# Performance work log

Hardware: AMD Instinct MI355X
Metric: run time of the kernel (lower is better)

## Reference

```python
import jax, jax.numpy as jnp
import numpy as np

NUM_NODES = 10000  # fixed by input spec: edge_index values in [0, 10000)


def setup_inputs() -> dict:
    key = jax.random.key(0)
    k1, k2, k3 = jax.random.split(key, 3)
    N, E, D_IN, D_OUT = NUM_NODES, 320000, 256, 256
    x = jax.random.normal(k1, (N, D_IN), dtype=jnp.float32)
    edge_index = jax.random.randint(k2, (2, E), 0, N, dtype=jnp.int64)
    # ensure node N-1 appears so num_nodes == N as in the torch code
    edge_index = edge_index.at[0, 0].set(N - 1)
    # xavier_uniform for [D_IN, D_OUT]
    limit = float(np.sqrt(6.0 / (D_IN + D_OUT)))
    weight = jax.random.uniform(k3, (D_IN, D_OUT), dtype=jnp.float32,
                                minval=-limit, maxval=limit)
    return {"x": x, "edge_index": edge_index, "weight": weight}


def _normalize_adjacency(edge_index, num_nodes):
    src, dst = edge_index[0], edge_index[1]
    ones = jnp.ones(src.shape[0], dtype=jnp.float32)
    # symmetric binarized adjacency: adj[i,j] = adj[j,i] = 1 (set, not add)
    adj = jnp.zeros((num_nodes, num_nodes), dtype=jnp.float32)
    adj = adj.at[src, dst].max(ones)
    adj = adj.at[dst, src].max(ones)
    # one round of self-loops: adj += I
    adj = adj + jnp.eye(num_nodes, dtype=jnp.float32)
    deg = jnp.sum(adj, axis=1)                    # [N]
    dinv = 1.0 / jnp.sqrt(deg)                    # [N]
    # D^-1/2 A D^-1/2 via broadcasting (equivalent to diag mms)
    return adj * dinv[:, None] * dinv[None, :]


def reference(x, edge_index, weight):
    adj = _normalize_adjacency(edge_index, NUM_NODES)  # [N, N]
    h = adj @ x                                        # [N, D_IN]
    return h @ weight                                  # [N, D_OUT]
```

## Files before the change

### kernel.cpp

```cpp
#include <hip/hip_runtime.h>
#include <hip/hip_bf16.h>
#include <stdint.h>

#define N_NODES   10000
#define D_FEAT    256
#define E_EDGES   320000
#define ROW_WORDS 313
#define ROW_STRIDE 320
#define LIST_CAP  1024

#define NB     1000
#define RPB    10
#define B_CAP  1024
#define NBLK_E 313
#define NBLK_W 64
#define NBLK_C 1000
#define NBLK_G 625
#define COLSTR 128

#define LDSTR 264

typedef __attribute__((ext_vector_type(4))) float float4v;
typedef _Float16 half8  __attribute__((ext_vector_type(8)));
typedef _Float16 half4v __attribute__((ext_vector_type(4)));

__device__ __forceinline__ float h2f_lo(uint32_t u) {
    union { uint32_t u; _Float16 h[2]; } v; v.u = u; return (float)v.h[0];
}
__device__ __forceinline__ float h2f_hi(uint32_t u) {
    union { uint32_t u; _Float16 h[2]; } v; v.u = u; return (float)v.h[1];
}


__global__ void __launch_bounds__(1024)
fill_sort(const int* __restrict__ ei, uint32_t* __restrict__ bucketbuf,
          uint32_t* __restrict__ cursors,
          const float* __restrict__ w, _Float16* __restrict__ wt) {
    __shared__ uint32_t hist[1024];
    __shared__ uint32_t lofs[1024];
    __shared__ uint32_t base_s[1024];
    __shared__ uint32_t wsum[16];
    __shared__ uint32_t stage[2048];
    __shared__ uint16_t sbkt[2048];
    int t = threadIdx.x;

    if (blockIdx.x >= NBLK_E) {
        int kb = (blockIdx.x - NBLK_E) * 4;
        int k = kb + (t >> 8), n = t & 255;
        float* st = (float*)stage;
        st[(n << 2) | (t >> 8)] = w[(size_t)k * D_FEAT + n];
        __syncthreads();
        if (t < 256) {
            half4v o = { (_Float16)st[t * 4 + 0], (_Float16)st[t * 4 + 1],
                         (_Float16)st[t * 4 + 2], (_Float16)st[t * 4 + 3] };
            *(half4v*)&wt[(size_t)t * D_FEAT + kb] = o;
        }
        return;
    }

    int wv = t >> 6, lane = t & 63;
    hist[t] = 0;
    __syncthreads();
    int e = blockIdx.x * 1024 + t;
    int b0 = -1, b1 = -1; uint32_t ent0 = 0, ent1 = 0, s0 = 0, s1 = 0;
    if (e < E_EDGES) {
        int s = ei[e], d = ei[E_EDGES + e];
        if ((uint32_t)s < N_NODES && (uint32_t)d < N_NODES) {
            b0 = s / RPB; ent0 = ((uint32_t)(s - b0 * RPB) << 14) | (uint32_t)d;
            b1 = d / RPB; ent1 = ((uint32_t)(d - b1 * RPB) << 14) | (uint32_t)s;
            s0 = atomicAdd(&hist[b0], 1u);
            s1 = atomicAdd(&hist[b1], 1u);
        }
    }
    __syncthreads();
    uint32_t h = hist[t];
    uint32_t incl = h;
    #pragma unroll
    for (int off = 1; off < 64; off <<= 1) {
        uint32_t v = __shfl_up(incl, off, 64);
        if (lane >= off) incl += v;
    }
    if (lane == 63) wsum[wv] = incl;
    __syncthreads();
    if (wv == 0) {
        uint32_t s = (lane < 16) ? wsum[lane] : 0u;
        #pragma unroll
        for (int off = 1; off < 16; off <<= 1) {
            uint32_t v = __shfl_up(s, off, 64);
            if (lane >= off) s += v;
        }
        if (lane < 16) wsum[lane] = s;
    }
    __syncthreads();
    uint32_t wbase = wv ? wsum[wv - 1] : 0u;
    lofs[t] = incl + wbase;
    base_s[t] = h ? atomicAdd(&cursors[t], h) : 0u;
    __syncthreads();
    if (b0 >= 0) {
        uint32_t p0 = lofs[b0] - hist[b0] + s0;
        stage[p0] = ent0; sbkt[p0] = (uint16_t)b0;
        uint32_t p1 = lofs[b1] - hist[b1] + s1;
        stage[p1] = ent1; sbkt[p1] = (uint16_t)b1;
    }
    __syncthreads();
    uint32_t total = lofs[1023];
    for (uint32_t idx = t; idx < total; idx += 1024) {
        uint32_t b = sbkt[idx];
        uint32_t pos = base_s[b] + (idx - (lofs[b] - hist[b]));
        if (pos < B_CAP) bucketbuf[(size_t)b * B_CAP + pos] = stage[idx];
    }
}

__global__ void __launch_bounds__(1024)
csr_gemm(const uint32_t* __restrict__ bucketbuf, const uint32_t* __restrict__ cursors,
         uint32_t* __restrict__ row_deg, float* __restrict__ dinv,
         uint16_t* __restrict__ col,
         const float* __restrict__ x, const _Float16* __restrict__ wt,
         _Float16* __restrict__ yw) {
    __shared__ __align__(16) uint32_t smem[RPB * ROW_WORDS];
    int t = threadIdx.x;

    if (blockIdx.x >= NBLK_C) {
        _Float16* a_lds = (_Float16*)smem;
        int r0 = (blockIdx.x - NBLK_C) * 16;
        int row = t >> 6, c4 = (t & 63) * 4;
        float4v xv = *(const float4v*)(x + (size_t)(r0 + row) * D_FEAT + c4);
        half4v h = { (_Float16)xv[0], (_Float16)xv[1],
                     (_Float16)xv[2], (_Float16)xv[3] };
        *(half4v*)&a_lds[row * LDSTR + c4] = h;
        __syncthreads();
        int wv = t >> 6, lane = t & 63;
        int quad = lane >> 4, r = lane & 15;
        int ct = wv;
        const _Float16* pb = wt + (size_t)(ct * 16 + r) * D_FEAT + quad * 8;
        float4v acc = {0.f, 0.f, 0.f, 0.f};
        #pragma unroll
        for (int kk = 0; kk < D_FEAT; kk += 32) {
            half8 a = *(const half8*)&a_lds[r * LDSTR + kk + quad * 8];
            half8 b = *(const half8*)(pb + kk);
            acc = __builtin_amdgcn_mfma_f32_16x16x32_f16(a, b, acc, 0, 0, 0);
        }
        int colg = ct * 16 + r;
        #pragma unroll
        for (int u = 0; u < 4; u++)
            yw[(size_t)(r0 + quad * 4 + u) * D_FEAT + colg] = (_Float16)acc[u];
        return;
    }

    uint32_t* bm = smem;
    int b = blockIdx.x;
    for (int i = t; i < RPB * ROW_WORDS; i += 1024) bm[i] = 0;
    __syncthreads();
    uint32_t cnt = min(cursors[b], (uint32_t)B_CAP);
    const uint32_t* bb = bucketbuf + (size_t)b * B_CAP;
    for (uint32_t i = t; i < cnt; i += 1024) {
        uint32_t ent = bb[i];
        uint32_t lr = ent >> 14, d = ent & 0x3FFFu;
        atomicOr(&bm[lr * ROW_WORDS + (d >> 5)], 1u << (d & 31));
    }
    __syncthreads();
    int wv = t >> 6, lane = t & 63;
    if (wv < RPB) {
        int r = wv;
        int gi = b * RPB + r;
        uint32_t wb[5]; int tot = 0;
        #pragma unroll
        for (int k = 0; k < 5; k++) {
            int w = lane + 64 * k;
            uint32_t v = (w < ROW_WORDS) ? bm[r * ROW_WORDS + w] : 0u;
            wb[k] = v; tot += __popc(v);
        }
        int incl = tot;
        #pragma unroll
        for (int off = 1; off < 64; off <<= 1) {
            int v = __shfl_up(incl, off, 64);
            if (lane >= off) incl += v;
        }
        uint32_t total = (uint32_t)__shfl(incl, 63, 64);
        if (lane == 0) {
            row_deg[gi] = min(total, (uint32_t)COLSTR);
            dinv[gi]    = 1.0f / sqrtf((float)(total + 1u));
        }
        uint32_t p = (uint32_t)(incl - tot);
        #pragma unroll
        for (int k = 0; k < 5; k++) {
            uint32_t bits = wb[k];
            uint32_t cbase = (uint32_t)(lane + 64 * k) << 5;
            while (bits) {
                if (p < COLSTR)
                    col[(size_t)gi * COLSTR + p] =
                        (uint16_t)(cbase + (uint32_t)__builtin_ctz(bits));
                p++;
                bits &= bits - 1;
            }
        }
    }
}

__global__ void __launch_bounds__(256)
spmm_out(const uint32_t* __restrict__ row_deg, const float* __restrict__ dinv,
         const uint16_t* __restrict__ col, const _Float16* __restrict__ ywp,
         float* __restrict__ out) {
    const uint16_t* yw = (const uint16_t*)ywp;
    int wv = threadIdx.x >> 6, lane = threadIdx.x & 63;
    int half = lane >> 5, sl = lane & 31;
    int i = blockIdx.x * 4 + wv;
    uint32_t base = (uint32_t)i * COLSTR;
    uint32_t deg = min(row_deg[i], (uint32_t)COLSTR);
    float di = dinv[i];
    size_t ch = (size_t)sl * 8;
    float4v z = {0.f, 0.f, 0.f, 0.f};
    float4v accl[8], acch[8];
    #pragma unroll
    for (int k = 0; k < 8; k++) { accl[k] = z; acch[k] = z; }

    uint32_t hb = (uint32_t)(half << 3);
    uint4 cv = {0u, 0u, 0u, 0u};
    if (deg) cv = *(const uint4*)&col[base + hb];

    for (uint32_t t = 0; t < deg; t += 16) {
        uint4 cvn = {0u, 0u, 0u, 0u};
        uint32_t tn = t + 16;
        if (tn < deg) cvn = *(const uint4*)&col[base + tn + hb];
        uint32_t tb = t + hb;
        uint32_t jr[8];
        jr[0] = cv.x & 0xffffu; jr[1] = cv.x >> 16;
        jr[2] = cv.y & 0xffffu; jr[3] = cv.y >> 16;
        jr[4] = cv.z & 0xffffu; jr[5] = cv.z >> 16;
        jr[6] = cv.w & 0xffffu; jr[7] = cv.w >> 16;
        uint4 g[8]; float dk[8];
        #pragma unroll
        for (int k = 0; k < 8; k++) {
            uint32_t j = min(jr[k], (uint32_t)(N_NODES - 1));
            g[k]  = *(const uint4*)(yw + ((size_t)j << 8) + ch);
            dk[k] = dinv[j];
        }
        #pragma unroll
        for (int k = 0; k < 8; k++) {
            float d = (tb + (uint32_t)k < deg) ? dk[k] : 0.f;
            accl[k][0] += d * h2f_lo(g[k].x); accl[k][1] += d * h2f_hi(g[k].x);
            accl[k][2] += d * h2f_lo(g[k].y); accl[k][3] += d * h2f_hi(g[k].y);
            acch[k][0] += d * h2f_lo(g[k].z); acch[k][1] += d * h2f_hi(g[k].z);
            acch[k][2] += d * h2f_lo(g[k].w); acch[k][3] += d * h2f_hi(g[k].w);
        }
        cv = cvn;
    }

    if (half == 0) {
        const uint4 gs = *(const uint4*)(yw + ((size_t)i << 8) + ch);
        accl[0][0] += di * h2f_lo(gs.x); accl[0][1] += di * h2f_hi(gs.x);
        accl[0][2] += di * h2f_lo(gs.y); accl[0][3] += di * h2f_hi(gs.y);
        acch[0][0] += di * h2f_lo(gs.z); acch[0][1] += di * h2f_hi(gs.z);
        acch[0][2] += di * h2f_lo(gs.w); acch[0][3] += di * h2f_hi(gs.w);
    }

    float4v lo = ((accl[0] + accl[1]) + (accl[2] + accl[3])) +
                 ((accl[4] + accl[5]) + (accl[6] + accl[7]));
    float4v hi = ((acch[0] + acch[1]) + (acch[2] + acch[3])) +
                 ((acch[4] + acch[5]) + (acch[6] + acch[7]));
    #pragma unroll
    for (int u = 0; u < 4; u++) {
        lo[u] += __shfl_xor(lo[u], 32, 64);
        hi[u] += __shfl_xor(hi[u], 32, 64);
    }
    float4v res;
    if (half) res = hi; else res = lo;
    float* op = out + (size_t)i * D_FEAT + (size_t)sl * 8 + (half ? 4 : 0);
    *(float4v*)op = di * res;
}


__global__ void scatter_edges_fb(const int* __restrict__ ei,
                                 uint32_t* __restrict__ bitmap) {
    int e = blockIdx.x * blockDim.x + threadIdx.x;
    if (e >= E_EDGES) return;
    int s = ei[e], d = ei[E_EDGES + e];
    if ((uint32_t)s >= N_NODES || (uint32_t)d >= N_NODES) return;
    atomicOr(&bitmap[(size_t)s * ROW_STRIDE + (d >> 5)], 1u << (d & 31));
    atomicOr(&bitmap[(size_t)d * ROW_STRIDE + (s >> 5)], 1u << (s & 31));
}

__global__ void __launch_bounds__(256)
popc_dinv(const uint32_t* __restrict__ bitmap, float* __restrict__ dinv) {
    int wv = threadIdx.x >> 6, lane = threadIdx.x & 63;
    int i = blockIdx.x * 4 + wv;
    const uint32_t* rb = bitmap + (size_t)i * ROW_STRIDE;
    int pop = 0;
    #pragma unroll
    for (int k = 0; k < 5; k++) {
        int w = lane + 64 * k;
        if (w < ROW_WORDS) pop += __popc(rb[w]);
    }
    #pragma unroll
    for (int off = 32; off > 0; off >>= 1) pop += __shfl_xor(pop, off, 64);
    if (lane == 0) dinv[i] = 1.0f / sqrtf((float)(pop + 1));
}

__global__ void __launch_bounds__(256)
spmm_bitmap_fb(const uint32_t* __restrict__ bitmap, const float* __restrict__ dinv,
               const float* __restrict__ xf, float* __restrict__ agg) {
    __shared__ __align__(16) uint32_t lists[4][LIST_CAP];
    int wv = threadIdx.x >> 6, lane = threadIdx.x & 63;
    int i = blockIdx.x * 4 + wv;
    uint32_t* list = lists[wv];
    const uint32_t* rb = bitmap + (size_t)i * ROW_STRIDE;

    uint32_t wbits[5]; int tot = 0;
    #pragma unroll
    for (int k = 0; k < 5; k++) {
        int w = lane + 64 * k;
        uint32_t b = (w < ROW_WORDS) ? rb[w] : 0u;
        wbits[k] = b;
        tot += __popc(b);
    }
    int incl = tot;
    #pragma unroll
    for (int off = 1; off < 64; off <<= 1) {
        int v = __shfl_up(incl, off, 64);
        if (lane >= off) incl += v;
    }
    uint32_t p = (uint32_t)(incl - tot);
    uint32_t deg = (uint32_t)__shfl(incl, 63, 64);
    #pragma unroll
    for (int k = 0; k < 5; k++) {
        uint32_t bits = wbits[k];
        uint32_t base = (uint32_t)(lane + 64 * k) << 5;
        while (bits) {
            if (p < LIST_CAP) list[p] = base + (uint32_t)__builtin_ctz(bits);
            p++;
            bits &= bits - 1;
        }
    }
    if (deg > LIST_CAP) deg = LIST_CAP;

    float di = dinv[i];
    float4v z = {0.f, 0.f, 0.f, 0.f};
    float4v acc0 = z, acc1 = z, acc2 = z, acc3 = z;
    float4v sv = *(const float4v*)(xf + (size_t)i * D_FEAT + lane * 4);
    uint32_t t4 = deg & ~3u;
    for (uint32_t k = 0; k < t4; k += 4) {
        uint4 jv = *(const uint4*)&list[k];
        float d0 = dinv[jv.x], d1 = dinv[jv.y], d2 = dinv[jv.z], d3 = dinv[jv.w];
        float4v v0 = *(const float4v*)(xf + (size_t)jv.x * D_FEAT + lane * 4);
        float4v v1 = *(const float4v*)(xf + (size_t)jv.y * D_FEAT + lane * 4);
        float4v v2 = *(const float4v*)(xf + (size_t)jv.z * D_FEAT + lane * 4);
        float4v v3 = *(const float4v*)(xf + (size_t)jv.w * D_FEAT + lane * 4);
        acc0 += d0 * v0; acc1 += d1 * v1; acc2 += d2 * v2; acc3 += d3 * v3;
    }
    for (uint32_t k = t4; k < deg; k++) {
        uint32_t j = list[k];
        acc0 += dinv[j] * (*(const float4v*)(xf + (size_t)j * D_FEAT + lane * 4));
    }
    float4v acc = (acc0 + acc1) + (acc2 + acc3) + di * sv;
    *(float4v*)(agg + (size_t)i * D_FEAT + lane * 4) = di * acc;
}

__global__ void __launch_bounds__(256)
gemm_valu(float* __restrict__ io, const float* __restrict__ wf) {
    __shared__ __align__(16) float a_lds[16 * D_FEAT];
    int c = threadIdx.x;
    int r0 = blockIdx.x * 16;
    for (int idx = c; idx < 16 * D_FEAT; idx += 256)
        a_lds[idx] = io[(size_t)r0 * D_FEAT + idx];
    __syncthreads();
    float acc[16];
    #pragma unroll
    for (int r = 0; r < 16; r++) acc[r] = 0.f;
    for (int k0 = 0; k0 < D_FEAT; k0 += 4) {
        float w0 = wf[(size_t)(k0 + 0) * D_FEAT + c];
        float w1 = wf[(size_t)(k0 + 1) * D_FEAT + c];
        float w2 = wf[(size_t)(k0 + 2) * D_FEAT + c];
        float w3 = wf[(size_t)(k0 + 3) * D_FEAT + c];
        #pragma unroll
        for (int r = 0; r < 16; r++) {
            float4v av = *(const float4v*)&a_lds[r * D_FEAT + k0];
            acc[r] = fmaf(av[3], w3, fmaf(av[2], w2,
                     fmaf(av[1], w1, fmaf(av[0], w0, acc[r]))));
        }
    }
    #pragma unroll
    for (int r = 0; r < 16; r++)
        io[(size_t)(r0 + r) * D_FEAT + c] = acc[r];
}

extern "C" void kernel_launch(void* const* d_in, const int* in_sizes, int n_in,
                              void* d_out, int out_size, void* d_ws, size_t ws_size,
                              hipStream_t stream) {
    const float* x  = (const float*)d_in[0];
    const int*   ei = (const int*)d_in[1];
    const float* w  = (const float*)d_in[2];
    float* out = (float*)d_out;
    uint8_t* ws = (uint8_t*)d_ws;

    const size_t BB_OFF   = 4096;
    const size_t RD_OFF   = 4100096;
    const size_t DI_OFF   = 4140096;
    const size_t WT_OFF   = 4180096;
    const size_t YW_OFF   = 4311168;
    const size_t COL_OFF  = 9431168;
    const size_t NEED_NEW = 11991168;
    const size_t NEED_FB  = 12840000;

    if (ws_size >= NEED_NEW) {
        uint32_t* cursors   = (uint32_t*)ws;
        uint32_t* bucketbuf = (uint32_t*)(ws + BB_OFF);
        uint32_t* row_deg   = (uint32_t*)(ws + RD_OFF);
        float*    dinv      = (float*)(ws + DI_OFF);
        _Float16* wt        = (_Float16*)(ws + WT_OFF);
        _Float16* yw        = (_Float16*)(ws + YW_OFF);
        uint16_t* col       = (uint16_t*)(ws + COL_OFF);

        hipMemsetAsync(cursors, 0, 4096, stream);
        fill_sort<<<NBLK_E + NBLK_W, 1024, 0, stream>>>(ei, bucketbuf, cursors, w, wt);
        csr_gemm <<<NBLK_C + NBLK_G, 1024, 0, stream>>>(bucketbuf, cursors,
                                                        row_deg, dinv, col, x, wt, yw);
        spmm_out <<<N_NODES / 4, 256, 0, stream>>>(row_deg, dinv, col, yw, out);
    } else if (ws_size >= NEED_FB) {
        uint32_t* bitmap = (uint32_t*)ws;
        float*    dinv   = (float*)(ws + 12800000);

        hipMemsetAsync(bitmap, 0, 12800000, stream);
        scatter_edges_fb<<<(E_EDGES + 255) / 256, 256, 0, stream>>>(ei, bitmap);
        popc_dinv      <<<N_NODES / 4, 256, 0, stream>>>(bitmap, dinv);
        spmm_bitmap_fb <<<N_NODES / 4, 256, 0, stream>>>(bitmap, dinv, x, out);
        gemm_valu      <<<N_NODES / 16, 256, 0, stream>>>(out, w);
    }
}
```

Before: 132.7 us.

## Add bitmap-adjacency path with fused weight cast and MFMA GEMM before SpMM

```diff
diff --git a/kernel.cpp b/kernel.cpp
--- a/kernel.cpp
+++ b/kernel.cpp
@@ -6,7 +6,6 @@
 #define D_FEAT    256
 #define E_EDGES   320000
 #define ROW_WORDS 313
-#define ROW_STRIDE 320
 #define LIST_CAP  1024
 
 #define NB     1000
@@ -29,6 +28,171 @@
 }
 __device__ __forceinline__ float h2f_hi(uint32_t u) {
     union { uint32_t u; _Float16 h[2]; } v; v.u = u; return (float)v.h[1];
+}
+
+
+__global__ void __launch_bounds__(1024)
+scatter_wcast(const int* __restrict__ ei, uint32_t* __restrict__ bitmap,
+              const float* __restrict__ w, _Float16* __restrict__ wt) {
+    __shared__ float st[1024];
+    int t = threadIdx.x;
+
+    if (blockIdx.x >= NBLK_E) {
+        int kb = (blockIdx.x - NBLK_E) * 4;
+        int k = kb + (t >> 8), n = t & 255;
+        st[(n << 2) | (t >> 8)] = w[(size_t)k * D_FEAT + n];
+        __syncthreads();
+        if (t < 256) {
+            half4v o = { (_Float16)st[t * 4 + 0], (_Float16)st[t * 4 + 1],
+                         (_Float16)st[t * 4 + 2], (_Float16)st[t * 4 + 3] };
+            *(half4v*)&wt[(size_t)t * D_FEAT + kb] = o;
+        }
+        return;
+    }
+
+    int e = blockIdx.x * 1024 + t;
+    if (e >= E_EDGES) return;
+    int s = ei[e], d = ei[E_EDGES + e];
+    if ((uint32_t)s >= N_NODES || (uint32_t)d >= N_NODES) return;
+    atomicOr(&bitmap[(size_t)s * ROW_WORDS + (d >> 5)], 1u << (d & 31));
+    atomicOr(&bitmap[(size_t)d * ROW_WORDS + (s >> 5)], 1u << (s & 31));
+}
+
+__global__ void __launch_bounds__(1024)
+gemm_popc(const uint32_t* __restrict__ bitmap, float* __restrict__ dinv,
+          const float* __restrict__ x, const _Float16* __restrict__ wt,
+          _Float16* __restrict__ yw) {
+    __shared__ __align__(16) _Float16 a_lds[16 * LDSTR];
+    int t = threadIdx.x;
+
+    if (blockIdx.x < NBLK_G) {
+        int r0 = blockIdx.x * 16;
+        int row = t >> 6, c4 = (t & 63) * 4;
+        float4v xv = *(const float4v*)(x + (size_t)(r0 + row) * D_FEAT + c4);
+        half4v h = { (_Float16)xv[0], (_Float16)xv[1],
+                     (_Float16)xv[2], (_Float16)xv[3] };
+        *(half4v*)&a_lds[row * LDSTR + c4] = h;
+        __syncthreads();
+        int wv = t >> 6, lane = t & 63;
+        int quad = lane >> 4, r = lane & 15;
+        int ct = wv;
+        const _Float16* pb = wt + (size_t)(ct * 16 + r) * D_FEAT + quad * 8;
+        float4v acc = {0.f, 0.f, 0.f, 0.f};
+        #pragma unroll
+        for (int kk = 0; kk < D_FEAT; kk += 32) {
+            half8 a = *(const half8*)&a_lds[r * LDSTR + kk + quad * 8];
+            half8 b = *(const half8*)(pb + kk);
+            acc = __builtin_amdgcn_mfma_f32_16x16x32_f16(a, b, acc, 0, 0, 0);
+        }
+        int colg = ct * 16 + r;
+        #pragma unroll
+        for (int u = 0; u < 4; u++)
+            yw[(size_t)(r0 + quad * 4 + u) * D_FEAT + colg] = (_Float16)acc[u];
+        return;
+    }
+
+    int wv = t >> 6, lane = t & 63;
+    int i = (blockIdx.x - NBLK_G) * 16 + wv;
+    const uint32_t* rb = bitmap + (size_t)i * ROW_WORDS;
+    int pop = 0;
+    #pragma unroll
+    for (int k = 0; k < 5; k++) {
+        int w = lane + 64 * k;
+        if (w < ROW_WORDS) pop += __popc(rb[w]);
+    }
+    #pragma unroll
+    for (int off = 32; off > 0; off >>= 1) pop += __shfl_xor(pop, off, 64);
+    if (lane == 0) dinv[i] = 1.0f / sqrtf((float)(pop + 1));
+}
+
+__global__ void __launch_bounds__(256)
+spmm_bm(const uint32_t* __restrict__ bitmap, const float* __restrict__ dinv,
+        const _Float16* __restrict__ ywp, float* __restrict__ out) {
+    __shared__ __align__(16) uint32_t lists[4][LIST_CAP];
+    const uint16_t* yw = (const uint16_t*)ywp;
+    int wv = threadIdx.x >> 6, lane = threadIdx.x & 63;
+    int i = blockIdx.x * 4 + wv;
+    uint32_t* list = lists[wv];
+    const uint32_t* rb = bitmap + (size_t)i * ROW_WORDS;
+
+    uint32_t wbits[5]; int tot = 0;
+    #pragma unroll
+    for (int k = 0; k < 5; k++) {
+        int w = lane + 64 * k;
+        uint32_t b = (w < ROW_WORDS) ? rb[w] : 0u;
+        wbits[k] = b;
+        tot += __popc(b);
+    }
+    int incl = tot;
+    #pragma unroll
+    for (int off = 1; off < 64; off <<= 1) {
+        int v = __shfl_up(incl, off, 64);
+        if (lane >= off) incl += v;
+    }
+    uint32_t p = (uint32_t)(incl - tot);
+    uint32_t deg = (uint32_t)__shfl(incl, 63, 64);
+    #pragma unroll
+    for (int k = 0; k < 5; k++) {
+        uint32_t bits = wbits[k];
+        uint32_t cbase = (uint32_t)(lane + 64 * k) << 5;
+        while (bits) {
+            if (p < LIST_CAP) list[p] = cbase + (uint32_t)__builtin_ctz(bits);
+            p++;
+            bits &= bits - 1;
+        }
+    }
+    if (deg > LIST_CAP) deg = LIST_CAP;
+
+    float di = dinv[i];
+    size_t ch = (size_t)lane * 4;
+    float4v z = {0.f, 0.f, 0.f, 0.f};
+    float4v a0 = z, a1 = z, a2 = z, a3 = z, a4 = z, a5 = z, a6 = z, a7 = z;
+    uint32_t t8 = deg & ~7u;
+    uint32_t t = 0;
+    for (; t < t8; t += 8) {
+        uint4 jv0 = *(const uint4*)&list[t];
+        uint4 jv1 = *(const uint4*)&list[t + 4];
+        uint32_t j0 = jv0.x, j1 = jv0.y, j2 = jv0.z, j3 = jv0.w;
+        uint32_t j4 = jv1.x, j5 = jv1.y, j6 = jv1.z, j7 = jv1.w;
+        float d0 = dinv[j0], d1 = dinv[j1], d2 = dinv[j2], d3 = dinv[j3];
+        float d4 = dinv[j4], d5 = dinv[j5], d6 = dinv[j6], d7 = dinv[j7];
+        uint2 g0 = *(const uint2*)(yw + (size_t)j0 * D_FEAT + ch);
+        uint2 g1 = *(const uint2*)(yw + (size_t)j1 * D_FEAT + ch);
+        uint2 g2 = *(const uint2*)(yw + (size_t)j2 * D_FEAT + ch);
+        uint2 g3 = *(const uint2*)(yw + (size_t)j3 * D_FEAT + ch);
+        uint2 g4 = *(const uint2*)(yw + (size_t)j4 * D_FEAT + ch);
+        uint2 g5 = *(const uint2*)(yw + (size_t)j5 * D_FEAT + ch);
+        uint2 g6 = *(const uint2*)(yw + (size_t)j6 * D_FEAT + ch);
+        uint2 g7 = *(const uint2*)(yw + (size_t)j7 * D_FEAT + ch);
+        a0[0] += d0 * h2f_lo(g0.x); a0[1] += d0 * h2f_hi(g0.x);
+        a0[2] += d0 * h2f_lo(g0.y); a0[3] += d0 * h2f_hi(g0.y);
+        a1[0] += d1 * h2f_lo(g1.x); a1[1] += d1 * h2f_hi(g1.x);
+        a1[2] += d1 * h2f_lo(g1.y); a1[3] += d1 * h2f_hi(g1.y);
+        a2[0] += d2 * h2f_lo(g2.x); a2[1] += d2 * h2f_hi(g2.x);
+        a2[2] += d2 * h2f_lo(g2.y); a2[3] += d2 * h2f_hi(g2.y);
+        a3[0] += d3 * h2f_lo(g3.x); a3[1] += d3 * h2f_hi(g3.x);
+        a3[2] += d3 * h2f_lo(g3.y); a3[3] += d3 * h2f_hi(g3.y);
+        a4[0] += d4 * h2f_lo(g4.x); a4[1] += d4 * h2f_hi(g4.x);
+        a4[2] += d4 * h2f_lo(g4.y); a4[3] += d4 * h2f_hi(g4.y);
+        a5[0] += d5 * h2f_lo(g5.x); a5[1] += d5 * h2f_hi(g5.x);
+        a5[2] += d5 * h2f_lo(g5.y); a5[3] += d5 * h2f_hi(g5.y);
+        a6[0] += d6 * h2f_lo(g6.x); a6[1] += d6 * h2f_hi(g6.x);
+        a6[2] += d6 * h2f_lo(g6.y); a6[3] += d6 * h2f_hi(g6.y);
+        a7[0] += d7 * h2f_lo(g7.x); a7[1] += d7 * h2f_hi(g7.x);
+        a7[2] += d7 * h2f_lo(g7.y); a7[3] += d7 * h2f_hi(g7.y);
+    }
+    for (; t < deg; t++) {
+        uint32_t j = list[t];
+        float dj = dinv[j];
+        uint2 g = *(const uint2*)(yw + (size_t)j * D_FEAT + ch);
+        a0[0] += dj * h2f_lo(g.x); a0[1] += dj * h2f_hi(g.x);
+        a0[2] += dj * h2f_lo(g.y); a0[3] += dj * h2f_hi(g.y);
+    }
+    uint2 gs = *(const uint2*)(yw + (size_t)i * D_FEAT + ch);
+    a1[0] += di * h2f_lo(gs.x); a1[1] += di * h2f_hi(gs.x);
+    a1[2] += di * h2f_lo(gs.y); a1[3] += di * h2f_hi(gs.y);
+    float4v acc = ((a0 + a1) + (a2 + a3)) + ((a4 + a5) + (a6 + a7));
+    *(float4v*)(out + (size_t)i * D_FEAT + ch) = di * acc;
 }
 
 
@@ -269,120 +433,6 @@
     *(float4v*)op = di * res;
 }
 
-
-__global__ void scatter_edges_fb(const int* __restrict__ ei,
-                                 uint32_t* __restrict__ bitmap) {
-    int e = blockIdx.x * blockDim.x + threadIdx.x;
-    if (e >= E_EDGES) return;
-    int s = ei[e], d = ei[E_EDGES + e];
-    if ((uint32_t)s >= N_NODES || (uint32_t)d >= N_NODES) return;
-    atomicOr(&bitmap[(size_t)s * ROW_STRIDE + (d >> 5)], 1u << (d & 31));
-    atomicOr(&bitmap[(size_t)d * ROW_STRIDE + (s >> 5)], 1u << (s & 31));
-}
-
-__global__ void __launch_bounds__(256)
-popc_dinv(const uint32_t* __restrict__ bitmap, float* __restrict__ dinv) {
-    int wv = threadIdx.x >> 6, lane = threadIdx.x & 63;
-    int i = blockIdx.x * 4 + wv;
-    const uint32_t* rb = bitmap + (size_t)i * ROW_STRIDE;
-    int pop = 0;
-    #pragma unroll
-    for (int k = 0; k < 5; k++) {
-        int w = lane + 64 * k;
-        if (w < ROW_WORDS) pop += __popc(rb[w]);
-    }
-    #pragma unroll
-    for (int off = 32; off > 0; off >>= 1) pop += __shfl_xor(pop, off, 64);
-    if (lane == 0) dinv[i] = 1.0f / sqrtf((float)(pop + 1));
-}
-
-__global__ void __launch_bounds__(256)
-spmm_bitmap_fb(const uint32_t* __restrict__ bitmap, const float* __restrict__ dinv,
-               const float* __restrict__ xf, float* __restrict__ agg) {
-    __shared__ __align__(16) uint32_t lists[4][LIST_CAP];
-    int wv = threadIdx.x >> 6, lane = threadIdx.x & 63;
-    int i = blockIdx.x * 4 + wv;
-    uint32_t* list = lists[wv];
-    const uint32_t* rb = bitmap + (size_t)i * ROW_STRIDE;
-
-    uint32_t wbits[5]; int tot = 0;
-    #pragma unroll
-    for (int k = 0; k < 5; k++) {
-        int w = lane + 64 * k;
-        uint32_t b = (w < ROW_WORDS) ? rb[w] : 0u;
-        wbits[k] = b;
-        tot += __popc(b);
-    }
-    int incl = tot;
-    #pragma unroll
-    for (int off = 1; off < 64; off <<= 1) {
-        int v = __shfl_up(incl, off, 64);
-        if (lane >= off) incl += v;
-    }
-    uint32_t p = (uint32_t)(incl - tot);
-    uint32_t deg = (uint32_t)__shfl(incl, 63, 64);
-    #pragma unroll
-    for (int k = 0; k < 5; k++) {
-        uint32_t bits = wbits[k];
-        uint32_t base = (uint32_t)(lane + 64 * k) << 5;
-        while (bits) {
-            if (p < LIST_CAP) list[p] = base + (uint32_t)__builtin_ctz(bits);
-            p++;
-            bits &= bits - 1;
-        }
-    }
-    if (deg > LIST_CAP) deg = LIST_CAP;
-
-    float di = dinv[i];
-    float4v z = {0.f, 0.f, 0.f, 0.f};
-    float4v acc0 = z, acc1 = z, acc2 = z, acc3 = z;
-    float4v sv = *(const float4v*)(xf + (size_t)i * D_FEAT + lane * 4);
-    uint32_t t4 = deg & ~3u;
-    for (uint32_t k = 0; k < t4; k += 4) {
-        uint4 jv = *(const uint4*)&list[k];
-        float d0 = dinv[jv.x], d1 = dinv[jv.y], d2 = dinv[jv.z], d3 = dinv[jv.w];
-        float4v v0 = *(const float4v*)(xf + (size_t)jv.x * D_FEAT + lane * 4);
-        float4v v1 = *(const float4v*)(xf + (size_t)jv.y * D_FEAT + lane * 4);
-        float4v v2 = *(const float4v*)(xf + (size_t)jv.z * D_FEAT + lane * 4);
-        float4v v3 = *(const float4v*)(xf + (size_t)jv.w * D_FEAT + lane * 4);
-        acc0 += d0 * v0; acc1 += d1 * v1; acc2 += d2 * v2; acc3 += d3 * v3;
-    }
-    for (uint32_t k = t4; k < deg; k++) {
-        uint32_t j = list[k];
-        acc0 += dinv[j] * (*(const float4v*)(xf + (size_t)j * D_FEAT + lane * 4));
-    }
-    float4v acc = (acc0 + acc1) + (acc2 + acc3) + di * sv;
-    *(float4v*)(agg + (size_t)i * D_FEAT + lane * 4) = di * acc;
-}
-
-__global__ void __launch_bounds__(256)
-gemm_valu(float* __restrict__ io, const float* __restrict__ wf) {
-    __shared__ __align__(16) float a_lds[16 * D_FEAT];
-    int c = threadIdx.x;
-    int r0 = blockIdx.x * 16;
-    for (int idx = c; idx < 16 * D_FEAT; idx += 256)
-        a_lds[idx] = io[(size_t)r0 * D_FEAT + idx];
-    __syncthreads();
-    float acc[16];
-    #pragma unroll
-    for (int r = 0; r < 16; r++) acc[r] = 0.f;
-    for (int k0 = 0; k0 < D_FEAT; k0 += 4) {
-        float w0 = wf[(size_t)(k0 + 0) * D_FEAT + c];
-        float w1 = wf[(size_t)(k0 + 1) * D_FEAT + c];
-        float w2 = wf[(size_t)(k0 + 2) * D_FEAT + c];
-        float w3 = wf[(size_t)(k0 + 3) * D_FEAT + c];
-        #pragma unroll
-        for (int r = 0; r < 16; r++) {
-            float4v av = *(const float4v*)&a_lds[r * D_FEAT + k0];
-            acc[r] = fmaf(av[3], w3, fmaf(av[2], w2,
-                     fmaf(av[1], w1, fmaf(av[0], w0, acc[r]))));
-        }
-    }
-    #pragma unroll
-    for (int r = 0; r < 16; r++)
-        io[(size_t)(r0 + r) * D_FEAT + c] = acc[r];
-}
-
 extern "C" void kernel_launch(void* const* d_in, const int* in_sizes, int n_in,
                               void* d_out, int out_size, void* d_ws, size_t ws_size,
                               hipStream_t stream) {
@@ -392,16 +442,30 @@
     float* out = (float*)d_out;
     uint8_t* ws = (uint8_t*)d_ws;
 
+    const size_t T1_DI   = 12520000;
+    const size_t T1_WT   = 12560000;
+    const size_t T1_YW   = 12691072;
+    const size_t NEED_T1 = 17811072;
+
     const size_t BB_OFF   = 4096;
     const size_t RD_OFF   = 4100096;
     const size_t DI_OFF   = 4140096;
     const size_t WT_OFF   = 4180096;
     const size_t YW_OFF   = 4311168;
     const size_t COL_OFF  = 9431168;
-    const size_t NEED_NEW = 11991168;
-    const size_t NEED_FB  = 12840000;
-
-    if (ws_size >= NEED_NEW) {
+    const size_t NEED_T2  = 11991168;
+
+    if (ws_size >= NEED_T1) {
+        uint32_t* bitmap = (uint32_t*)ws;
+        float*    dinv   = (float*)(ws + T1_DI);
+        _Float16* wt     = (_Float16*)(ws + T1_WT);
+        _Float16* yw     = (_Float16*)(ws + T1_YW);
+
+        hipMemsetAsync(bitmap, 0, 12520000, stream);
+        scatter_wcast<<<NBLK_E + NBLK_W, 1024, 0, stream>>>(ei, bitmap, w, wt);
+        gemm_popc    <<<NBLK_G + 625, 1024, 0, stream>>>(bitmap, dinv, x, wt, yw);
+        spmm_bm      <<<N_NODES / 4, 256, 0, stream>>>(bitmap, dinv, yw, out);
+    } else if (ws_size >= NEED_T2) {
         uint32_t* cursors   = (uint32_t*)ws;
         uint32_t* bucketbuf = (uint32_t*)(ws + BB_OFF);
         uint32_t* row_deg   = (uint32_t*)(ws + RD_OFF);
@@ -415,14 +479,5 @@
         csr_gemm <<<NBLK_C + NBLK_G, 1024, 0, stream>>>(bucketbuf, cursors,
                                                         row_deg, dinv, col, x, wt, yw);
         spmm_out <<<N_NODES / 4, 256, 0, stream>>>(row_deg, dinv, col, yw, out);
-    } else if (ws_size >= NEED_FB) {
-        uint32_t* bitmap = (uint32_t*)ws;
-        float*    dinv   = (float*)(ws + 12800000);
-
-        hipMemsetAsync(bitmap, 0, 12800000, stream);
-        scatter_edges_fb<<<(E_EDGES + 255) / 256, 256, 0, stream>>>(ei, bitmap);
-        popc_dinv      <<<N_NODES / 4, 256, 0, stream>>>(bitmap, dinv);
-        spmm_bitmap_fb <<<N_NODES / 4, 256, 0, stream>>>(bitmap, dinv, x, out);
-        gemm_valu      <<<N_NODES / 16, 256, 0, stream>>>(out, w);
-    }
-}
+    }
+}
```

Measured after the change: 140.4 us. +5.8%, slower.

## Move X·W GEMM blocks into the sort kernel and split out weight cast

Applied to the files above, without the earlier changes.

```diff
diff --git a/kernel.cpp b/kernel.cpp
--- a/kernel.cpp
+++ b/kernel.cpp
@@ -6,16 +6,13 @@
 #define D_FEAT    256
 #define E_EDGES   320000
 #define ROW_WORDS 313
-#define ROW_STRIDE 320
-#define LIST_CAP  1024
 
 #define NB     1000
 #define RPB    10
 #define B_CAP  1024
 #define NBLK_E 313
-#define NBLK_W 64
+#define NBLK_G 625
 #define NBLK_C 1000
-#define NBLK_G 625
 #define COLSTR 128
 
 #define LDSTR 264
@@ -33,32 +30,62 @@
 
 
 __global__ void __launch_bounds__(1024)
-fill_sort(const int* __restrict__ ei, uint32_t* __restrict__ bucketbuf,
+wcast_k(const float* __restrict__ w, _Float16* __restrict__ wt) {
+    __shared__ float st[1024];
+    int t = threadIdx.x;
+    int kb = blockIdx.x * 4;
+    int k = kb + (t >> 8), n = t & 255;
+    st[(n << 2) | (t >> 8)] = w[(size_t)k * D_FEAT + n];
+    __syncthreads();
+    if (t < 256) {
+        half4v o = { (_Float16)st[t * 4 + 0], (_Float16)st[t * 4 + 1],
+                     (_Float16)st[t * 4 + 2], (_Float16)st[t * 4 + 3] };
+        *(half4v*)&wt[(size_t)t * D_FEAT + kb] = o;
+    }
+}
+
+__global__ void __launch_bounds__(1024)
+sort_gemm(const int* __restrict__ ei, uint32_t* __restrict__ bucketbuf,
           uint32_t* __restrict__ cursors,
-          const float* __restrict__ w, _Float16* __restrict__ wt) {
-    __shared__ uint32_t hist[1024];
-    __shared__ uint32_t lofs[1024];
-    __shared__ uint32_t base_s[1024];
-    __shared__ uint32_t wsum[16];
-    __shared__ uint32_t stage[2048];
-    __shared__ uint16_t sbkt[2048];
+          const float* __restrict__ x, const _Float16* __restrict__ wt,
+          _Float16* __restrict__ yw) {
+    __shared__ __align__(16) uint8_t smraw[24640];
     int t = threadIdx.x;
+    int wv = t >> 6, lane = t & 63;
 
     if (blockIdx.x >= NBLK_E) {
-        int kb = (blockIdx.x - NBLK_E) * 4;
-        int k = kb + (t >> 8), n = t & 255;
-        float* st = (float*)stage;
-        st[(n << 2) | (t >> 8)] = w[(size_t)k * D_FEAT + n];
+        _Float16* a_lds = (_Float16*)smraw;
+        int r0 = (blockIdx.x - NBLK_E) * 16;
+        int row = t >> 6, c4 = (t & 63) * 4;
+        float4v xv = *(const float4v*)(x + (size_t)(r0 + row) * D_FEAT + c4);
+        half4v h = { (_Float16)xv[0], (_Float16)xv[1],
+                     (_Float16)xv[2], (_Float16)xv[3] };
+        *(half4v*)&a_lds[row * LDSTR + c4] = h;
         __syncthreads();
-        if (t < 256) {
-            half4v o = { (_Float16)st[t * 4 + 0], (_Float16)st[t * 4 + 1],
-                         (_Float16)st[t * 4 + 2], (_Float16)st[t * 4 + 3] };
-            *(half4v*)&wt[(size_t)t * D_FEAT + kb] = o;
-        }
+        int quad = lane >> 4, r = lane & 15;
+        int ct = wv;
+        const _Float16* pb = wt + (size_t)(ct * 16 + r) * D_FEAT + quad * 8;
+        float4v acc = {0.f, 0.f, 0.f, 0.f};
+        #pragma unroll
+        for (int kk = 0; kk < D_FEAT; kk += 32) {
+            half8 a = *(const half8*)&a_lds[r * LDSTR + kk + quad * 8];
+            half8 b = *(const half8*)(pb + kk);
+            acc = __builtin_amdgcn_mfma_f32_16x16x32_f16(a, b, acc, 0, 0, 0);
+        }
+        int colg = ct * 16 + r;
+        #pragma unroll
+        for (int u = 0; u < 4; u++)
+            yw[(size_t)(r0 + quad * 4 + u) * D_FEAT + colg] = (_Float16)acc[u];
         return;
     }
 
-    int wv = t >> 6, lane = t & 63;
+    uint32_t* hist   = (uint32_t*)(smraw);
+    uint32_t* lofs   = (uint32_t*)(smraw + 4096);
+    uint32_t* base_s = (uint32_t*)(smraw + 8192);
+    uint32_t* wsum   = (uint32_t*)(smraw + 12288);
+    uint32_t* stage  = (uint32_t*)(smraw + 12352);
+    uint16_t* sbkt   = (uint16_t*)(smraw + 20544);
+
     hist[t] = 0;
     __syncthreads();
     int e = blockIdx.x * 1024 + t;
@@ -112,42 +139,11 @@
 }
 
 __global__ void __launch_bounds__(1024)
-csr_gemm(const uint32_t* __restrict__ bucketbuf, const uint32_t* __restrict__ cursors,
+csr_only(const uint32_t* __restrict__ bucketbuf, const uint32_t* __restrict__ cursors,
          uint32_t* __restrict__ row_deg, float* __restrict__ dinv,
-         uint16_t* __restrict__ col,
-         const float* __restrict__ x, const _Float16* __restrict__ wt,
-         _Float16* __restrict__ yw) {
-    __shared__ __align__(16) uint32_t smem[RPB * ROW_WORDS];
+         uint16_t* __restrict__ col) {
+    __shared__ __align__(16) uint32_t bm[RPB * ROW_WORDS];
     int t = threadIdx.x;
-
-    if (blockIdx.x >= NBLK_C) {
-        _Float16* a_lds = (_Float16*)smem;
-        int r0 = (blockIdx.x - NBLK_C) * 16;
-        int row = t >> 6, c4 = (t & 63) * 4;
-        float4v xv = *(const float4v*)(x + (size_t)(r0 + row) * D_FEAT + c4);
-        half4v h = { (_Float16)xv[0], (_Float16)xv[1],
-                     (_Float16)xv[2], (_Float16)xv[3] };
-        *(half4v*)&a_lds[row * LDSTR + c4] = h;
-        __syncthreads();
-        int wv = t >> 6, lane = t & 63;
-        int quad = lane >> 4, r = lane & 15;
-        int ct = wv;
-        const _Float16* pb = wt + (size_t)(ct * 16 + r) * D_FEAT + quad * 8;
-        float4v acc = {0.f, 0.f, 0.f, 0.f};
-        #pragma unroll
-        for (int kk = 0; kk < D_FEAT; kk += 32) {
-            half8 a = *(const half8*)&a_lds[r * LDSTR + kk + quad * 8];
-            half8 b = *(const half8*)(pb + kk);
-            acc = __builtin_amdgcn_mfma_f32_16x16x32_f16(a, b, acc, 0, 0, 0);
-        }
-        int colg = ct * 16 + r;
-        #pragma unroll
-        for (int u = 0; u < 4; u++)
-            yw[(size_t)(r0 + quad * 4 + u) * D_FEAT + colg] = (_Float16)acc[u];
-        return;
-    }
-
-    uint32_t* bm = smem;
     int b = blockIdx.x;
     for (int i = t; i < RPB * ROW_WORDS; i += 1024) bm[i] = 0;
     __syncthreads();
@@ -269,120 +265,6 @@
     *(float4v*)op = di * res;
 }
 
-
-__global__ void scatter_edges_fb(const int* __restrict__ ei,
-                                 uint32_t* __restrict__ bitmap) {
-    int e = blockIdx.x * blockDim.x + threadIdx.x;
-    if (e >= E_EDGES) return;
-    int s = ei[e], d = ei[E_EDGES + e];
-    if ((uint32_t)s >= N_NODES || (uint32_t)d >= N_NODES) return;
-    atomicOr(&bitmap[(size_t)s * ROW_STRIDE + (d >> 5)], 1u << (d & 31));
-    atomicOr(&bitmap[(size_t)d * ROW_STRIDE + (s >> 5)], 1u << (s & 31));
-}
-
-__global__ void __launch_bounds__(256)
-popc_dinv(const uint32_t* __restrict__ bitmap, float* __restrict__ dinv) {
-    int wv = threadIdx.x >> 6, lane = threadIdx.x & 63;
-    int i = blockIdx.x * 4 + wv;
-    const uint32_t* rb = bitmap + (size_t)i * ROW_STRIDE;
-    int pop = 0;
-    #pragma unroll
-    for (int k = 0; k < 5; k++) {
-        int w = lane + 64 * k;
-        if (w < ROW_WORDS) pop += __popc(rb[w]);
-    }
-    #pragma unroll
-    for (int off = 32; off > 0; off >>= 1) pop += __shfl_xor(pop, off, 64);
-    if (lane == 0) dinv[i] = 1.0f / sqrtf((float)(pop + 1));
-}
-
-__global__ void __launch_bounds__(256)
-spmm_bitmap_fb(const uint32_t* __restrict__ bitmap, const float* __restrict__ dinv,
-               const float* __restrict__ xf, float* __restrict__ agg) {
-    __shared__ __align__(16) uint32_t lists[4][LIST_CAP];
-    int wv = threadIdx.x >> 6, lane = threadIdx.x & 63;
-    int i = blockIdx.x * 4 + wv;
-    uint32_t* list = lists[wv];
-    const uint32_t* rb = bitmap + (size_t)i * ROW_STRIDE;
-
-    uint32_t wbits[5]; int tot = 0;
-    #pragma unroll
-    for (int k = 0; k < 5; k++) {
-        int w = lane + 64 * k;
-        uint32_t b = (w < ROW_WORDS) ? rb[w] : 0u;
-        wbits[k] = b;
-        tot += __popc(b);
-    }
-    int incl = tot;
-    #pragma unroll
-    for (int off = 1; off < 64; off <<= 1) {
-        int v = __shfl_up(incl, off, 64);
-        if (lane >= off) incl += v;
-    }
-    uint32_t p = (uint32_t)(incl - tot);
-    uint32_t deg = (uint32_t)__shfl(incl, 63, 64);
-    #pragma unroll
-    for (int k = 0; k < 5; k++) {
-        uint32_t bits = wbits[k];
-        uint32_t base = (uint32_t)(lane + 64 * k) << 5;
-        while (bits) {
-            if (p < LIST_CAP) list[p] = base + (uint32_t)__builtin_ctz(bits);
-            p++;
-            bits &= bits - 1;
-        }
-    }
-    if (deg > LIST_CAP) deg = LIST_CAP;
-
-    float di = dinv[i];
-    float4v z = {0.f, 0.f, 0.f, 0.f};
-    float4v acc0 = z, acc1 = z, acc2 = z, acc3 = z;
-    float4v sv = *(const float4v*)(xf + (size_t)i * D_FEAT + lane * 4);
-    uint32_t t4 = deg & ~3u;
-    for (uint32_t k = 0; k < t4; k += 4) {
-        uint4 jv = *(const uint4*)&list[k];
-        float d0 = dinv[jv.x], d1 = dinv[jv.y], d2 = dinv[jv.z], d3 = dinv[jv.w];
-        float4v v0 = *(const float4v*)(xf + (size_t)jv.x * D_FEAT + lane * 4);
-        float4v v1 = *(const float4v*)(xf + (size_t)jv.y * D_FEAT + lane * 4);
-        float4v v2 = *(const float4v*)(xf + (size_t)jv.z * D_FEAT + lane * 4);
-        float4v v3 = *(const float4v*)(xf + (size_t)jv.w * D_FEAT + lane * 4);
-        acc0 += d0 * v0; acc1 += d1 * v1; acc2 += d2 * v2; acc3 += d3 * v3;
-    }
-    for (uint32_t k = t4; k < deg; k++) {
-        uint32_t j = list[k];
-        acc0 += dinv[j] * (*(const float4v*)(xf + (size_t)j * D_FEAT + lane * 4));
-    }
-    float4v acc = (acc0 + acc1) + (acc2 + acc3) + di * sv;
-    *(float4v*)(agg + (size_t)i * D_FEAT + lane * 4) = di * acc;
-}
-
-__global__ void __launch_bounds__(256)
-gemm_valu(float* __restrict__ io, const float* __restrict__ wf) {
-    __shared__ __align__(16) float a_lds[16 * D_FEAT];
-    int c = threadIdx.x;
-    int r0 = blockIdx.x * 16;
-    for (int idx = c; idx < 16 * D_FEAT; idx += 256)
-        a_lds[idx] = io[(size_t)r0 * D_FEAT + idx];
-    __syncthreads();
-    float acc[16];
-    #pragma unroll
-    for (int r = 0; r < 16; r++) acc[r] = 0.f;
-    for (int k0 = 0; k0 < D_FEAT; k0 += 4) {
-        float w0 = wf[(size_t)(k0 + 0) * D_FEAT + c];
-        float w1 = wf[(size_t)(k0 + 1) * D_FEAT + c];
-        float w2 = wf[(size_t)(k0 + 2) * D_FEAT + c];
-        float w3 = wf[(size_t)(k0 + 3) * D_FEAT + c];
-        #pragma unroll
-        for (int r = 0; r < 16; r++) {
-            float4v av = *(const float4v*)&a_lds[r * D_FEAT + k0];
-            acc[r] = fmaf(av[3], w3, fmaf(av[2], w2,
-                     fmaf(av[1], w1, fmaf(av[0], w0, acc[r]))));
-        }
-    }
-    #pragma unroll
-    for (int r = 0; r < 16; r++)
-        io[(size_t)(r0 + r) * D_FEAT + c] = acc[r];
-}
-
 extern "C" void kernel_launch(void* const* d_in, const int* in_sizes, int n_in,
                               void* d_out, int out_size, void* d_ws, size_t ws_size,
                               hipStream_t stream) {
@@ -398,31 +280,23 @@
     const size_t WT_OFF   = 4180096;
     const size_t YW_OFF   = 4311168;
     const size_t COL_OFF  = 9431168;
-    const size_t NEED_NEW = 11991168;
-    const size_t NEED_FB  = 12840000;
-
-    if (ws_size >= NEED_NEW) {
-        uint32_t* cursors   = (uint32_t*)ws;
-        uint32_t* bucketbuf = (uint32_t*)(ws + BB_OFF);
-        uint32_t* row_deg   = (uint32_t*)(ws + RD_OFF);
-        float*    dinv      = (float*)(ws + DI_OFF);
-        _Float16* wt        = (_Float16*)(ws + WT_OFF);
-        _Float16* yw        = (_Float16*)(ws + YW_OFF);
-        uint16_t* col       = (uint16_t*)(ws + COL_OFF);
-
-        hipMemsetAsync(cursors, 0, 4096, stream);
-        fill_sort<<<NBLK_E + NBLK_W, 1024, 0, stream>>>(ei, bucketbuf, cursors, w, wt);
-        csr_gemm <<<NBLK_C + NBLK_G, 1024, 0, stream>>>(bucketbuf, cursors,
-                                                        row_deg, dinv, col, x, wt, yw);
-        spmm_out <<<N_NODES / 4, 256, 0, stream>>>(row_deg, dinv, col, yw, out);
-    } else if (ws_size >= NEED_FB) {
-        uint32_t* bitmap = (uint32_t*)ws;
-        float*    dinv   = (float*)(ws + 12800000);
-
-        hipMemsetAsync(bitmap, 0, 12800000, stream);
-        scatter_edges_fb<<<(E_EDGES + 255) / 256, 256, 0, stream>>>(ei, bitmap);
-        popc_dinv      <<<N_NODES / 4, 256, 0, stream>>>(bitmap, dinv);
-        spmm_bitmap_fb <<<N_NODES / 4, 256, 0, stream>>>(bitmap, dinv, x, out);
-        gemm_valu      <<<N_NODES / 16, 256, 0, stream>>>(out, w);
-    }
-}
+    const size_t NEED     = 11991168;
+
+    if (ws_size < NEED) return;
+
+    uint32_t* cursors   = (uint32_t*)ws;
+    uint32_t* bucketbuf = (uint32_t*)(ws + BB_OFF);
+    uint32_t* row_deg   = (uint32_t*)(ws + RD_OFF);
+    float*    dinv      = (float*)(ws + DI_OFF);
+    _Float16* wt        = (_Float16*)(ws + WT_OFF);
+    _Float16* yw        = (_Float16*)(ws + YW_OFF);
+    uint16_t* col       = (uint16_t*)(ws + COL_OFF);
+
+    hipMemsetAsync(cursors, 0, 4096, stream);
+    wcast_k  <<<64, 1024, 0, stream>>>(w, wt);
+    sort_gemm<<<NBLK_E + NBLK_G, 1024, 0, stream>>>(ei, bucketbuf, cursors,
+                                                    x, wt, yw);
+    csr_only <<<NBLK_C, 1024, 0, stream>>>(bucketbuf, cursors,
+                                           row_deg, dinv, col);
+    spmm_out <<<N_NODES / 4, 256, 0, stream>>>(row_deg, dinv, col, yw, out);
+}
```

Result: no change. 131.2 us (-1.1%).
